# Optimization experiments

Hardware: AMD Instinct MI355X
Metric: run time of the kernel (lower is better)

Reference implementation:

```python
import jax, jax.numpy as jnp
import numpy as np

D_MODEL = 1024
N_HEADS = 16
D_K = D_MODEL // N_HEADS
B, L = 4, 2048


def setup_inputs() -> dict:
    key = jax.random.key(0)
    ks = jax.random.split(key, 9)
    s = 1.0 / np.sqrt(D_MODEL)
    return {
        "x": jax.random.normal(ks[0], (B, L, D_MODEL), dtype=jnp.float32),
        "Wq": jax.random.normal(ks[1], (D_MODEL, D_MODEL), dtype=jnp.float32) * s,
        "bq": jax.random.normal(ks[2], (D_MODEL,), dtype=jnp.float32) * 0.01,
        "Wk": jax.random.normal(ks[3], (D_MODEL, D_MODEL), dtype=jnp.float32) * s,
        "bk": jax.random.normal(ks[4], (D_MODEL,), dtype=jnp.float32) * 0.01,
        "Wv": jax.random.normal(ks[5], (D_MODEL, D_MODEL), dtype=jnp.float32) * s,
        "bv": jax.random.normal(ks[6], (D_MODEL,), dtype=jnp.float32) * 0.01,
        "Wo": jax.random.normal(ks[7], (D_MODEL, D_MODEL), dtype=jnp.float32) * s,
        "bo": jax.random.normal(ks[8], (D_MODEL,), dtype=jnp.float32) * 0.01,
    }


def reference(x, Wq, bq, Wk, bk, Wv, bv, Wo, bo):
    b, l, d = x.shape
    scale = jnp.asarray(np.sqrt(D_K), x.dtype)
    # project and split heads: [B, H, L, d_k]
    def heads(w, bias):
        p = x @ w.T + bias
        return p.reshape(b, l, N_HEADS, D_K).transpose(0, 2, 1, 3)
    Q = heads(Wq, bq)
    K = heads(Wk, bk)
    V = heads(Wv, bv)
    scores = jnp.einsum("bhqd,bhkd->bhqk", Q, K) / scale
    scores = jnp.clip(scores, -100.0, 100.0)
    attn = jax.nn.softmax(scores, axis=-1)  # dropout is identity in eval
    ctx = jnp.einsum("bhqk,bhkd->bhqd", attn, V)
    ctx = ctx.transpose(0, 2, 1, 3).reshape(b, l, d)
    return ctx @ Wo.T + bo
```

## Files before the change

kernel.cpp:

```cpp
#include <hip/hip_runtime.h>
#include <stdint.h>

#define L_SEQ   2048
#define DM      1024
#define NH      16
#define DK      64
#define BATCH   4
#define M_TOK   (BATCH * L_SEQ)

typedef __attribute__((ext_vector_type(8))) short bf16x8;
typedef __attribute__((ext_vector_type(4))) float f32x4;
typedef __attribute__((ext_vector_type(16))) float f32x16;
typedef __attribute__((ext_vector_type(4))) unsigned int u32x4;

typedef __attribute__((address_space(1))) void void_g;
typedef __attribute__((address_space(3))) void void_l;

#define EXP2F(x) __builtin_amdgcn_exp2f(x)

__device__ __forceinline__ unsigned short f2bf(float f) {
  unsigned int u = __builtin_bit_cast(unsigned int, f);
  u += 0x7FFFu + ((u >> 16) & 1u);
  return (unsigned short)(u >> 16);
}

__global__ void cvt_f32_bf16(const float* __restrict__ src,
                             unsigned short* __restrict__ dst, int n4) {
  int i = blockIdx.x * blockDim.x + threadIdx.x;
  int stride = gridDim.x * blockDim.x;
  for (; i < n4; i += stride) {
    float4 v = ((const float4*)src)[i];
    ushort4 o;
    o.x = f2bf(v.x); o.y = f2bf(v.y); o.z = f2bf(v.z); o.w = f2bf(v.w);
    ((ushort4*)dst)[i] = o;
  }
}

__global__ void cvt_w4(const float* __restrict__ s0, const float* __restrict__ s1,
                       const float* __restrict__ s2, const float* __restrict__ s3,
                       unsigned short* __restrict__ dst) {
  int i = blockIdx.x * blockDim.x + threadIdx.x;
  int sel = i >> 18, j = i & 0x3FFFF;
  const float* s = sel == 0 ? s0 : sel == 1 ? s1 : sel == 2 ? s2 : s3;
  float4 v = ((const float4*)s)[j];
  ushort4 o;
  o.x = f2bf(v.x); o.y = f2bf(v.y); o.z = f2bf(v.z); o.w = f2bf(v.w);
  ((ushort4*)(dst + (size_t)sel * DM * DM))[j] = o;
}

#define GBK 32
#define NKT (DM / GBK)
#define AT32 (128 * GBK)

template <int NW, int NCH>
__device__ __forceinline__ void stage32(
    const unsigned short* __restrict__ S, unsigned short* buf,
    int row0, int k0, int t) {
  const int l = t & 63, w = t >> 6;
  const int su = (l & 3) ^ ((l >> 3) & 3);
  const int rl = l >> 2;
#pragma unroll
  for (int r = 0; r < NCH / NW; ++r) {
    const int c = r * NW + w;
    __builtin_amdgcn_global_load_lds(
        (const void_g*)(S + (size_t)(row0 + c * 16 + rl) * DM + k0 + su * 8),
        (void_l*)(buf + c * 512), 16, 0, 0);
  }
}

__device__ __forceinline__ bf16x8 frag_ld32(const unsigned short* base, int R, int u) {
  return *(const bf16x8*)(base + R * 32 + ((u ^ ((R >> 1) & 3)) * 8));
}

template <int EPI, int BN_, int NW>
__global__ __launch_bounds__(NW * 64, EPI == 0 ? 4 : 3) void gemm8(
    const unsigned short* __restrict__ A,
    const unsigned short* __restrict__ Bw,
    const float* __restrict__ b0, const float* __restrict__ b1,
    const float* __restrict__ b2, float qscale,
    void* __restrict__ out) {
  constexpr int BUFE = (128 + BN_) * GBK;
  constexpr int BCH = BN_ / 16;
  __shared__ unsigned short L[3 * BUFE];

  const int tidx = threadIdx.x;
  const int wid = tidx >> 6, lane = tidx & 63;
  constexpr int WN = NW / 2;
  const int wm = wid / WN, wn = wid % WN;
  const int lr = lane & 15, lg4 = lane >> 4;

  int wg = blockIdx.y * gridDim.x + blockIdx.x;
  int nwg = gridDim.x * gridDim.y;
  int swz = (wg & 7) * (nwg >> 3) + (wg >> 3);
  const int tm = (swz / gridDim.x) * 128, tn = (swz % gridDim.x) * BN_;

  f32x4 acc[4][4];
#pragma unroll
  for (int m = 0; m < 4; ++m)
#pragma unroll
    for (int n = 0; n < 4; ++n) acc[m][n] = (f32x4)0.0f;

  stage32<NW, 8>(A, L, tm, 0, tidx);
  stage32<NW, BCH>(Bw, L + AT32, tn, 0, tidx);
  stage32<NW, 8>(A, L + BUFE, tm, GBK, tidx);
  stage32<NW, BCH>(Bw, L + BUFE + AT32, tn, GBK, tidx);
  if constexpr (EPI == 0) asm volatile("s_waitcnt vmcnt(3)" ::: "memory");
  else                    asm volatile("s_waitcnt vmcnt(4)" ::: "memory");
  __builtin_amdgcn_s_barrier();

  for (int i = 0; i < NKT; ++i) {
    unsigned short* cb = L + (i % 3) * BUFE;
    unsigned short* nb = L + ((i + 2) % 3) * BUFE;
    const bool pf = (i + 2 < NKT);

    bf16x8 a[4], b[4];
#pragma unroll
    for (int m = 0; m < 4; ++m)
      a[m] = frag_ld32(cb, wm * 64 + m * 16 + lr, lg4);
#pragma unroll
    for (int n = 0; n < 4; ++n)
      b[n] = frag_ld32(cb + AT32, wn * 64 + n * 16 + lr, lg4);

    if (pf) {
      stage32<NW, 8>(A, nb, tm, (i + 2) * GBK, tidx);
      stage32<NW, BCH>(Bw, nb + AT32, tn, (i + 2) * GBK, tidx);
    }

    asm volatile("s_waitcnt lgkmcnt(0)" ::: "memory");
    __builtin_amdgcn_s_setprio(1);
#pragma unroll
    for (int m = 0; m < 4; ++m)
#pragma unroll
      for (int n = 0; n < 4; ++n)
        acc[m][n] = __builtin_amdgcn_mfma_f32_16x16x32_bf16(a[m], b[n], acc[m][n], 0, 0, 0);
    __builtin_amdgcn_s_setprio(0);

    if (pf) {
      if constexpr (EPI == 0) asm volatile("s_waitcnt vmcnt(3)" ::: "memory");
      else                    asm volatile("s_waitcnt vmcnt(4)" ::: "memory");
    } else {
      asm volatile("s_waitcnt vmcnt(0)" ::: "memory");
    }
    __builtin_amdgcn_s_barrier();
  }

  if (EPI == 1) {
    float* o = (float*)out;
#pragma unroll
    for (int m = 0; m < 4; ++m) {
      int row0 = tm + wm * 64 + m * 16 + lg4 * 4;
#pragma unroll
      for (int n = 0; n < 4; ++n) {
        int col = tn + wn * 64 + n * 16 + lr;
        float bc = b0[col];
#pragma unroll
        for (int jj = 0; jj < 4; ++jj)
          o[(size_t)(row0 + jj) * DM + col] = acc[m][n][jj] + bc;
      }
    }
  } else {
    const int sel = tn >> 10;
    const float* bias = sel == 0 ? b0 : sel == 1 ? b1 : b2;
    const float scl = sel == 0 ? qscale : 1.0f;
    unsigned short* dst = (unsigned short*)out + (size_t)sel * (8u << 20);
    unsigned short* C = L;
    const int bb = tm >> 11, l0 = tm & 2047;
    const int tnl = tn & 1023;

    if (sel < 2) {
#pragma unroll
      for (int m = 0; m < 4; ++m) {
        int row0 = wm * 64 + m * 16 + lg4 * 4;
#pragma unroll
        for (int n = 0; n < 4; ++n) {
          int col = wn * 64 + n * 16 + lr;
          float bc = bias[tnl + col];
#pragma unroll
          for (int jj = 0; jj < 4; ++jj)
            C[(row0 + jj) * 264 + col] = f2bf((acc[m][n][jj] + bc) * scl);
        }
      }
      __syncthreads();
#pragma unroll
      for (int j = 0; j < 8; ++j) {
        int c = j * 512 + tidx;
        int ll = c >> 5, colc = (c & 31) * 8;
        bf16x8 v = *(const bf16x8*)&C[ll * 264 + colc];
        int c10 = tnl + colc;
        int h = c10 >> 6, dd = c10 & 63;
        *(bf16x8*)&dst[(((size_t)bb * NH + h) * L_SEQ + (l0 + ll)) * DK + dd] = v;
      }
    } else {
#pragma unroll
      for (int m = 0; m < 4; ++m) {
        int row0 = wm * 64 + m * 16 + lg4 * 4;
#pragma unroll
        for (int n = 0; n < 4; ++n) {
          int col = wn * 64 + n * 16 + lr;
          float bc = bias[tnl + col];
          ushort4 pk;
          pk.x = f2bf(acc[m][n][0] + bc);
          pk.y = f2bf(acc[m][n][1] + bc);
          pk.z = f2bf(acc[m][n][2] + bc);
          pk.w = f2bf(acc[m][n][3] + bc);
          *(ushort4*)&C[col * 136 + row0] = pk;
        }
      }
      __syncthreads();
#pragma unroll
      for (int j = 0; j < 8; ++j) {
        int c = j * 512 + tidx;
        int ddl = c >> 4, tk = (c & 15) * 8;
        bf16x8 v = *(const bf16x8*)&C[ddl * 136 + tk];
        int c10 = tnl + ddl;
        int h = c10 >> 6, dd = c10 & 63;
        *(bf16x8*)&dst[(((size_t)bb * NH + h) * DK + dd) * L_SEQ + (l0 + tk)] = v;
      }
    }
  }
}

#define KVB 64
#define LDK 68
#define NTILE (L_SEQ / KVB)
#define FIXM  32.0f

__device__ __forceinline__ bf16x8 lds_frag(const unsigned short* p) {
  uint2 a = *(const uint2*)p;
  uint2 b = *(const uint2*)(p + 4);
  u32x4 t = {a.x, a.y, b.x, b.y};
  return __builtin_bit_cast(bf16x8, t);
}

__device__ __forceinline__ void lds_st16(unsigned short* p, uint4 v) {
  *(uint2*)p = make_uint2(v.x, v.y);
  *(uint2*)(p + 4) = make_uint2(v.z, v.w);
}

__device__ __forceinline__ unsigned cvtpk(float a, float b) {
  unsigned r;
  asm("v_cvt_pk_bf16_f32 %0, %1, %2" : "=v"(r) : "v"(a), "v"(b));
  return r;
}

__device__ __forceinline__ void pl32swap(unsigned& a, unsigned& b) {
  unsigned sa = (unsigned)__shfl_xor((int)a, 32);
  unsigned sb = (unsigned)__shfl_xor((int)b, 32);
  int hi = (threadIdx.x & 63) >> 5;
  unsigned na = hi ? sb : a;
  unsigned nb = hi ? b : sa;
  a = na; b = nb;
}

__device__ __forceinline__ void xpair32(float x, float& lo, float& hi2) {
  unsigned a = __builtin_bit_cast(unsigned, x), b = a;
  pl32swap(a, b);
  lo = __builtin_bit_cast(float, a);
  hi2 = __builtin_bit_cast(float, b);
}

#define MFMA32(a, b, c) __builtin_amdgcn_mfma_f32_32x32x16_bf16(a, b, c, 0, 0, 0)

__global__ __launch_bounds__(256, 4) void flash_attn(
    const unsigned short* __restrict__ Qg,
    const unsigned short* __restrict__ Kg,
    const unsigned short* __restrict__ VTg,
    unsigned short* __restrict__ ctx, int bh0) {
  __shared__ unsigned short Ks[2][64 * LDK];
  __shared__ unsigned short Vs[2][64 * LDK];

  const int bh = blockIdx.x + bh0, b = bh >> 4, h = bh & 15;
  const int q0 = blockIdx.y * 128;
  const int tid = threadIdx.x;
  const int w = tid >> 6, lane = tid & 63;
  const int l31 = lane & 31, hi = lane >> 5;
  const size_t head = (size_t)bh * (L_SEQ * DK);

  const int srow = w * 16 + (lane >> 2);
  const int scol = (lane & 3) * 16;

  bf16x8 qf[4];
  {
    const unsigned short* qp = Qg + head + (size_t)(q0 + w * 32 + l31) * DK + hi * 8;
#pragma unroll
    for (int ks = 0; ks < 4; ++ks) qf[ks] = *(const bf16x8*)(qp + ks * 16);
  }

  f32x16 o[2];
  o[0] = (f32x16)0.0f; o[1] = (f32x16)0.0f;
  float lq = 0.0f;

  {
    const unsigned short* kp = Kg + head + (size_t)srow * DK + scol;
    uint4 k0 = *(const uint4*)kp, k1 = *(const uint4*)(kp + 8);
    const unsigned short* vp = VTg + head + (size_t)srow * L_SEQ + scol;
    uint4 v0 = *(const uint4*)vp, v1 = *(const uint4*)(vp + 8);
    lds_st16(Ks[0] + srow * LDK + scol, k0);
    lds_st16(Ks[0] + srow * LDK + scol + 8, k1);
    lds_st16(Vs[0] + srow * LDK + scol, v0);
    lds_st16(Vs[0] + srow * LDK + scol + 8, v1);
  }
  __syncthreads();

  int cur = 0;
  for (int t = 0; t < NTILE; ++t) {
    uint4 kr0, kr1, vr0, vr1;
    const int kv0n = (t + 1) * KVB;
    if (t + 1 < NTILE) {
      const unsigned short* kp = Kg + head + (size_t)(kv0n + srow) * DK + scol;
      kr0 = *(const uint4*)kp; kr1 = *(const uint4*)(kp + 8);
    }

    f32x16 s0 = (f32x16)(-FIXM), s1 = (f32x16)(-FIXM);
#pragma unroll
    for (int ks = 0; ks < 4; ++ks) {
      bf16x8 k0 = lds_frag(Ks[cur] + l31 * LDK + ks * 16 + hi * 8);
      s0 = MFMA32(k0, qf[ks], s0);
      bf16x8 k1 = lds_frag(Ks[cur] + (32 + l31) * LDK + ks * 16 + hi * 8);
      s1 = MFMA32(k1, qf[ks], s1);
    }

#pragma unroll
    for (int r = 0; r < 16; ++r) {
      s0[r] = EXP2F(s0[r]);
      s1[r] = EXP2F(s1[r]);
    }
    {
      float l4[4];
#pragma unroll
      for (int r = 0; r < 4; ++r)
        l4[r] = ((s0[r] + s0[r + 4]) + (s0[r + 8] + s0[r + 12]))
              + ((s1[r] + s1[r + 4]) + (s1[r + 8] + s1[r + 12]));
      lq += (l4[0] + l4[1]) + (l4[2] + l4[3]);
    }

    bf16x8 pa[4];
#pragma unroll
    for (int ks = 0; ks < 4; ++ks) {
      const int s8 = (ks & 1) * 8;
      const f32x16 sv = (ks < 2) ? s0 : s1;
      unsigned uA0 = cvtpk(sv[s8 + 0], sv[s8 + 1]);
      unsigned uA1 = cvtpk(sv[s8 + 2], sv[s8 + 3]);
      unsigned uB0 = cvtpk(sv[s8 + 4], sv[s8 + 5]);
      unsigned uB1 = cvtpk(sv[s8 + 6], sv[s8 + 7]);
      pl32swap(uA0, uB0);
      pl32swap(uA1, uB1);
      u32x4 tt = {uA0, uA1, uB0, uB1};
      pa[ks] = __builtin_bit_cast(bf16x8, tt);
    }

    if (t + 1 < NTILE) {
      const unsigned short* vp = VTg + head + (size_t)srow * L_SEQ + kv0n + scol;
      vr0 = *(const uint4*)vp; vr1 = *(const uint4*)(vp + 8);
    }

#pragma unroll
    for (int jb = 0; jb < 2; ++jb)
#pragma unroll
      for (int ks = 0; ks < 4; ++ks) {
        bf16x8 vf = lds_frag(Vs[cur] + (32 * jb + l31) * LDK + ks * 16 + hi * 8);
        o[jb] = MFMA32(vf, pa[ks], o[jb]);
      }

    if (t + 1 < NTILE) {
      lds_st16(Ks[cur ^ 1] + srow * LDK + scol, kr0);
      lds_st16(Ks[cur ^ 1] + srow * LDK + scol + 8, kr1);
      lds_st16(Vs[cur ^ 1] + srow * LDK + scol, vr0);
      lds_st16(Vs[cur ^ 1] + srow * LDK + scol + 8, vr1);
    }
    __syncthreads();
    cur ^= 1;
  }

  {
    float a, c;
    xpair32(lq, a, c);
    float inv = 1.0f / (a + c);
    const int tok = q0 + w * 32 + l31;
    size_t base = ((size_t)b * L_SEQ + tok) * DM + h * DK;
#pragma unroll
    for (int jb = 0; jb < 2; ++jb)
#pragma unroll
      for (int c2 = 0; c2 < 4; ++c2) {
        ushort4 pk;
        pk.x = f2bf(o[jb][4 * c2 + 0] * inv);
        pk.y = f2bf(o[jb][4 * c2 + 1] * inv);
        pk.z = f2bf(o[jb][4 * c2 + 2] * inv);
        pk.w = f2bf(o[jb][4 * c2 + 3] * inv);
        *(ushort4*)&ctx[base + jb * 32 + c2 * 8 + hi * 4] = pk;
      }
  }
}

extern "C" void kernel_launch(void* const* d_in, const int* in_sizes, int n_in,
                              void* d_out, int out_size, void* d_ws, size_t ws_size,
                              hipStream_t stream) {
  (void)in_sizes; (void)n_in; (void)out_size; (void)ws_size;
  const float* x  = (const float*)d_in[0];
  const float* Wq = (const float*)d_in[1];
  const float* bq = (const float*)d_in[2];
  const float* Wk = (const float*)d_in[3];
  const float* bk = (const float*)d_in[4];
  const float* Wv = (const float*)d_in[5];
  const float* bv = (const float*)d_in[6];
  const float* Wo = (const float*)d_in[7];
  const float* bo = (const float*)d_in[8];

  char* ws = (char*)d_ws;
  unsigned short* xb  = (unsigned short*)(ws);
  unsigned short* wqb = (unsigned short*)(ws + (16ull << 20));
  unsigned short* wob = (unsigned short*)(ws + (22ull << 20));
  unsigned short* Qb  = (unsigned short*)(ws + (24ull << 20));
  unsigned short* Kb  = (unsigned short*)(ws + (40ull << 20));
  unsigned short* VTb = (unsigned short*)(ws + (56ull << 20));
  unsigned short* ctx = xb;

  cvt_f32_bf16<<<2048, 256, 0, stream>>>(x, xb, M_TOK * DM / 4);
  cvt_w4<<<4096, 256, 0, stream>>>(Wq, Wk, Wv, Wo, wqb);

  gemm8<0, 256, 8><<<dim3(3 * DM / 256, M_TOK / 128), 512, 0, stream>>>(
      xb, wqb, bq, bk, bv, 0.1803368801f, Qb);

  dim3 ga(BATCH * NH / 2, L_SEQ / 128);
  flash_attn<<<ga, 256, 0, stream>>>(Qb, Kb, VTb, ctx, 0);
  flash_attn<<<ga, 256, 0, stream>>>(Qb, Kb, VTb, ctx, 32);

  gemm8<1, 128, 4><<<dim3(DM / 128, M_TOK / 128), 256, 0, stream>>>(
      ctx, wob, bo, nullptr, nullptr, 1.0f, d_out);
}
```

Measured before the change: 195.7 us.

## Double-buffer QKV GEMM LDS, split epilogue in halves, merge attention launches

The QKV projection GEMM moves from a triple-buffered to a double-buffered LDS ring, with prefetch distance 2 kept. The next tile is now written into the buffer just read, guarded by an extra barrier, and the launch-bounds occupancy hint rises. The epilogue transposes and stores the output tile in two halves so its staging buffer fits in the smaller LDS. The two half-grid flash-attention launches are merged into one full-grid launch. The aim is more resident blocks per CU and less launch overhead, at the cost of an extra barrier per K-step and possible register pressure from the tighter launch bound.

```diff
diff --git a/kernel.cpp b/kernel.cpp
--- a/kernel.cpp
+++ b/kernel.cpp
@@ -72,8 +72,8 @@
   return *(const bf16x8*)(base + R * 32 + ((u ^ ((R >> 1) & 3)) * 8));
 }
 
-template <int EPI, int BN_, int NW>
-__global__ __launch_bounds__(NW * 64, EPI == 0 ? 4 : 3) void gemm8(
+template <int EPI, int BN_, int NW, int NBUF>
+__global__ __launch_bounds__(NW * 64, NBUF == 2 ? 6 : 3) void gemm8(
     const unsigned short* __restrict__ A,
     const unsigned short* __restrict__ Bw,
     const float* __restrict__ b0, const float* __restrict__ b1,
@@ -81,7 +81,7 @@
     void* __restrict__ out) {
   constexpr int BUFE = (128 + BN_) * GBK;
   constexpr int BCH = BN_ / 16;
-  __shared__ unsigned short L[3 * BUFE];
+  __shared__ unsigned short L[NBUF * BUFE];
 
   const int tidx = threadIdx.x;
   const int wid = tidx >> 6, lane = tidx & 63;
@@ -109,8 +109,8 @@
   __builtin_amdgcn_s_barrier();
 
   for (int i = 0; i < NKT; ++i) {
-    unsigned short* cb = L + (i % 3) * BUFE;
-    unsigned short* nb = L + ((i + 2) % 3) * BUFE;
+    unsigned short* cb = L + (NBUF == 2 ? (i & 1) : (i % 3)) * BUFE;
+    unsigned short* nb = NBUF == 2 ? cb : L + ((i + 2) % 3) * BUFE;
     const bool pf = (i + 2 < NKT);
 
     bf16x8 a[4], b[4];
@@ -120,13 +120,19 @@
 #pragma unroll
     for (int n = 0; n < 4; ++n)
       b[n] = frag_ld32(cb + AT32, wn * 64 + n * 16 + lr, lg4);
+
+    if constexpr (NBUF == 2) {
+      asm volatile("s_waitcnt lgkmcnt(0)" ::: "memory");
+      __builtin_amdgcn_s_barrier();
+    }
 
     if (pf) {
       stage32<NW, 8>(A, nb, tm, (i + 2) * GBK, tidx);
       stage32<NW, BCH>(Bw, nb + AT32, tn, (i + 2) * GBK, tidx);
     }
 
-    asm volatile("s_waitcnt lgkmcnt(0)" ::: "memory");
+    if constexpr (NBUF == 3)
+      asm volatile("s_waitcnt lgkmcnt(0)" ::: "memory");
     __builtin_amdgcn_s_setprio(1);
 #pragma unroll
     for (int m = 0; m < 4; ++m)
@@ -169,52 +175,64 @@
 
     if (sel < 2) {
 #pragma unroll
-      for (int m = 0; m < 4; ++m) {
-        int row0 = wm * 64 + m * 16 + lg4 * 4;
-#pragma unroll
-        for (int n = 0; n < 4; ++n) {
-          int col = wn * 64 + n * 16 + lr;
-          float bc = bias[tnl + col];
-#pragma unroll
-          for (int jj = 0; jj < 4; ++jj)
-            C[(row0 + jj) * 264 + col] = f2bf((acc[m][n][jj] + bc) * scl);
+      for (int half = 0; half < 2; ++half) {
+        if (wm == half) {
+#pragma unroll
+          for (int m = 0; m < 4; ++m) {
+            int rl = m * 16 + lg4 * 4;
+#pragma unroll
+            for (int n = 0; n < 4; ++n) {
+              int col = wn * 64 + n * 16 + lr;
+              float bc = bias[tnl + col];
+#pragma unroll
+              for (int jj = 0; jj < 4; ++jj)
+                C[(rl + jj) * 264 + col] = f2bf((acc[m][n][jj] + bc) * scl);
+            }
+          }
         }
-      }
-      __syncthreads();
-#pragma unroll
-      for (int j = 0; j < 8; ++j) {
-        int c = j * 512 + tidx;
-        int ll = c >> 5, colc = (c & 31) * 8;
-        bf16x8 v = *(const bf16x8*)&C[ll * 264 + colc];
-        int c10 = tnl + colc;
-        int h = c10 >> 6, dd = c10 & 63;
-        *(bf16x8*)&dst[(((size_t)bb * NH + h) * L_SEQ + (l0 + ll)) * DK + dd] = v;
+        __syncthreads();
+#pragma unroll
+        for (int j = 0; j < 4; ++j) {
+          int c = j * 512 + tidx;
+          int ll = c >> 5, colc = (c & 31) * 8;
+          bf16x8 v = *(const bf16x8*)&C[ll * 264 + colc];
+          int c10 = tnl + colc;
+          int h = c10 >> 6, dd = c10 & 63;
+          *(bf16x8*)&dst[(((size_t)bb * NH + h) * L_SEQ + (l0 + half * 64 + ll)) * DK + dd] = v;
+        }
+        __syncthreads();
       }
     } else {
 #pragma unroll
-      for (int m = 0; m < 4; ++m) {
-        int row0 = wm * 64 + m * 16 + lg4 * 4;
-#pragma unroll
-        for (int n = 0; n < 4; ++n) {
-          int col = wn * 64 + n * 16 + lr;
-          float bc = bias[tnl + col];
-          ushort4 pk;
-          pk.x = f2bf(acc[m][n][0] + bc);
-          pk.y = f2bf(acc[m][n][1] + bc);
-          pk.z = f2bf(acc[m][n][2] + bc);
-          pk.w = f2bf(acc[m][n][3] + bc);
-          *(ushort4*)&C[col * 136 + row0] = pk;
+      for (int half = 0; half < 2; ++half) {
+        if ((wn >> 1) == half) {
+#pragma unroll
+          for (int m = 0; m < 4; ++m) {
+            int row0 = wm * 64 + m * 16 + lg4 * 4;
+#pragma unroll
+            for (int n = 0; n < 4; ++n) {
+              int cl = (wn & 1) * 64 + n * 16 + lr;
+              float bc = bias[tnl + half * 128 + cl];
+              ushort4 pk;
+              pk.x = f2bf(acc[m][n][0] + bc);
+              pk.y = f2bf(acc[m][n][1] + bc);
+              pk.z = f2bf(acc[m][n][2] + bc);
+              pk.w = f2bf(acc[m][n][3] + bc);
+              *(ushort4*)&C[cl * 136 + row0] = pk;
+            }
+          }
         }
-      }
-      __syncthreads();
-#pragma unroll
-      for (int j = 0; j < 8; ++j) {
-        int c = j * 512 + tidx;
-        int ddl = c >> 4, tk = (c & 15) * 8;
-        bf16x8 v = *(const bf16x8*)&C[ddl * 136 + tk];
-        int c10 = tnl + ddl;
-        int h = c10 >> 6, dd = c10 & 63;
-        *(bf16x8*)&dst[(((size_t)bb * NH + h) * DK + dd) * L_SEQ + (l0 + tk)] = v;
+        __syncthreads();
+#pragma unroll
+        for (int j = 0; j < 4; ++j) {
+          int c = j * 512 + tidx;
+          int ddl = c >> 4, tk = (c & 15) * 8;
+          bf16x8 v = *(const bf16x8*)&C[ddl * 136 + tk];
+          int c10 = tnl + half * 128 + ddl;
+          int h = c10 >> 6, dd = c10 & 63;
+          *(bf16x8*)&dst[(((size_t)bb * NH + h) * DK + dd) * L_SEQ + (l0 + tk)] = v;
+        }
+        __syncthreads();
       }
     }
   }
@@ -265,11 +283,11 @@
     const unsigned short* __restrict__ Qg,
     const unsigned short* __restrict__ Kg,
     const unsigned short* __restrict__ VTg,
-    unsigned short* __restrict__ ctx, int bh0) {
+    unsigned short* __restrict__ ctx) {
   __shared__ unsigned short Ks[2][64 * LDK];
   __shared__ unsigned short Vs[2][64 * LDK];
 
-  const int bh = blockIdx.x + bh0, b = bh >> 4, h = bh & 15;
+  const int bh = blockIdx.x, b = bh >> 4, h = bh & 15;
   const int q0 = blockIdx.y * 128;
   const int tid = threadIdx.x;
   const int w = tid >> 6, lane = tid & 63;
@@ -418,13 +436,12 @@
   cvt_f32_bf16<<<2048, 256, 0, stream>>>(x, xb, M_TOK * DM / 4);
   cvt_w4<<<4096, 256, 0, stream>>>(Wq, Wk, Wv, Wo, wqb);
 
-  gemm8<0, 256, 8><<<dim3(3 * DM / 256, M_TOK / 128), 512, 0, stream>>>(
+  gemm8<0, 256, 8, 2><<<dim3(3 * DM / 256, M_TOK / 128), 512, 0, stream>>>(
       xb, wqb, bq, bk, bv, 0.1803368801f, Qb);
 
-  dim3 ga(BATCH * NH / 2, L_SEQ / 128);
-  flash_attn<<<ga, 256, 0, stream>>>(Qb, Kb, VTb, ctx, 0);
-  flash_attn<<<ga, 256, 0, stream>>>(Qb, Kb, VTb, ctx, 32);
-
-  gemm8<1, 128, 4><<<dim3(DM / 128, M_TOK / 128), 256, 0, stream>>>(
+  dim3 ga(BATCH * NH, L_SEQ / 128);
+  flash_attn<<<ga, 256, 0, stream>>>(Qb, Kb, VTb, ctx);
+
+  gemm8<1, 128, 4, 3><<<dim3(DM / 128, M_TOK / 128), 256, 0, stream>>>(
       ctx, wob, bo, nullptr, nullptr, 1.0f, d_out);
 }
```

Result: slower. 613.1 us (+213.3%).
